# Kernel tuning notes

Measured on AMD Instinct MI355X. Metric: run time of the kernel, lower is better.

The kernel has to match this reference:

```python
import jax, jax.numpy as jnp
import numpy as np

D_MODEL = 512
EPS = 1e-5


def setup_inputs() -> dict:
    key = jax.random.key(0)
    k1, k2, k3 = jax.random.split(key, 3)
    B, N, D = 8, 2048, D_MODEL
    output = jax.random.normal(k1, (B, N, D), dtype=jnp.float32)
    # multiplicative 0/1 float mask over the [B, N, N] score matrix
    slf_attn_mask = jax.random.randint(k2, (B, N, N), 0, 2).astype(jnp.float32)
    # nn.Linear(d_model, d_model): weight [out, in], xavier-uniform; bias zeros-ish
    limit = float(np.sqrt(6.0 / (D + D)))
    W = jax.random.uniform(k3, (D, D), dtype=jnp.float32, minval=-limit, maxval=limit)
    b = jnp.zeros((D,), dtype=jnp.float32)
    return {"output": output, "slf_attn_mask": slf_attn_mask, "W": W, "b": b}


def reference(output, slf_attn_mask, W, b):
    temperature = jnp.asarray(D_MODEL, output.dtype) ** 0.5
    # scores: [B, N, N] = (q / temp) @ k^T, then multiplicative mask
    attn = jnp.einsum("bnd,bmd->bnm", output / temperature, output) * slf_attn_mask
    # F.normalize(p=2, dim=-1, eps=1e-5): x / max(||x||_2, eps)
    norm = jnp.sqrt(jnp.sum(attn * attn, axis=-1, keepdims=True))
    attn = attn / jnp.maximum(norm, EPS)
    # values: elu(Linear(output)), Linear uses W @ x + b with W [out, in]
    v = jax.nn.elu(jnp.einsum("bnd,ed->bne", output, W) + b)
    return jnp.einsum("bnm,bme->bne", attn, v)
```

## Files before the change

kernel.cpp:

```cpp
#include <hip/hip_runtime.h>
#include <hip/hip_bf16.h>

#define NSEQ 2048
#define DM 512
#define BATCH 8
#define GTOT (BATCH * NSEQ)
#define INV_T 0.044194173824159216f
#define EPSN 1e-5f

typedef __bf16 bf16_t;
typedef bf16_t bf16x8 __attribute__((ext_vector_type(8)));
typedef float f32x16 __attribute__((ext_vector_type(16)));
typedef unsigned short u16;
typedef unsigned int u32;
typedef unsigned long long u64;

__device__ __forceinline__ u16 f2bf(float f) {
    u32 u = __builtin_bit_cast(u32, f);
    u32 r = (u + 0x7FFFu + ((u >> 16) & 1u)) >> 16;
    return (u16)r;
}

__device__ __forceinline__ void async16(const u16* g, u16* l) {
    __builtin_amdgcn_global_load_lds(
        (const __attribute__((address_space(1))) u32*)g,
        (__attribute__((address_space(3))) u32*)l, 16, 0, 0);
}

__device__ __forceinline__ bf16x8 fragld64(const u16* t, int row, int kc) {
    return *(const bf16x8*)(t + row * 64 + ((kc ^ ((row >> 1) & 7)) << 3));
}

#define MFMA32(a, b, c) __builtin_amdgcn_mfma_f32_32x32x16_bf16(a, b, c, 0, 0, 0)
#define ROWOFF(reg, lh) (((reg) & 3) + 8 * ((reg) >> 2) + 4 * (lh))

#define STAGE64(Ag, ldA, Bg, ldB, k0)                                            \
    do {                                                                         \
        _Pragma("unroll") for (int j = 0; j < 4; ++j) {                          \
            const int cg = (lane & 7) ^ ((j * 4 + (lane >> 4)) & 7);             \
            const int dst = (wave * 4 + j) * 512 + lane * 8;                     \
            async16((Ag) + (long)(rS + j * 8) * (ldA) + (k0) + cg * 8, Ab + dst);\
            async16((Bg) + (long)(rS + j * 8) * (ldB) + (k0) + cg * 8, Bb + dst);\
        }                                                                        \
    } while (0)

__global__ __launch_bounds__(256) void k_convert(
    const float* __restrict__ X, const float* __restrict__ W,
    const float* __restrict__ mask, u16* __restrict__ Kbf, u16* __restrict__ Wbf,
    u64* __restrict__ Mbits, float* __restrict__ ssbuf) {
    const int bid = blockIdx.x;
    if (bid < 32768) {
        const int w = threadIdx.x >> 6, lane = threadIdx.x & 63;
        float4 f = ((const float4*)mask)[(long)bid * 256 + threadIdx.x];
        u64 b0 = __ballot(f.x != 0.f);
        u64 b1 = __ballot(f.y != 0.f);
        u64 b2 = __ballot(f.z != 0.f);
        u64 b3 = __ballot(f.w != 0.f);
        if (lane == 0) {
            u64* p = Mbits + ((long)bid * 4 + w) * 4;
            ((ulonglong2*)p)[0] = (ulonglong2){b0, b1};
            ((ulonglong2*)p)[1] = (ulonglong2){b2, b3};
        }
        return;
    }
    const long NK = (long)GTOT * DM / 4;
    const long NW = (long)DM * DM / 4;
    const long NS = GTOT / 4;
    long i = (long)(bid - 32768) * 256 + threadIdx.x;
    if (i < NK) {
        float4 f = ((const float4*)X)[i];
        ushort4 o;
        o.x = f2bf(f.x); o.y = f2bf(f.y); o.z = f2bf(f.z); o.w = f2bf(f.w);
        ((ushort4*)Kbf)[i] = o;
    } else if (i < NK + NW) {
        long j = i - NK;
        float4 f = ((const float4*)W)[j];
        ushort4 o;
        o.x = f2bf(f.x); o.y = f2bf(f.y); o.z = f2bf(f.z); o.w = f2bf(f.w);
        ((ushort4*)Wbf)[j] = o;
    } else if (i < NK + NW + NS) {
        ((float4*)ssbuf)[i - NK - NW] = (float4){0.f, 0.f, 0.f, 0.f};
    }
}

__global__ __launch_bounds__(256, 4) void k_sgemm(
    const u16* __restrict__ Kbf, const u64* __restrict__ Mbits,
    u16* __restrict__ Sbuf, float* __restrict__ ssbuf) {
    __shared__ __attribute__((aligned(16))) u16 Ab[8192], Bb[8192];
    const int tid = threadIdx.x, wave = tid >> 6, lane = tid & 63;
    const int l31 = lane & 31, lh = lane >> 5;
    const int wy = wave >> 1, wx = wave & 1;
    const int bid = blockIdx.x;
    const int b = bid & 7;
    const int ty = (bid >> 3) & 15, tx = bid >> 7;
    const int M0 = ty * 128, N0 = tx * 128;
    const u16* Ag = Kbf + (long)(b * NSEQ + M0) * DM;
    const u16* Bg = Kbf + (long)(b * NSEQ + N0) * DM;

    const int rS = wave * 32 + (lane >> 3);

    f32x16 acc[2][2];
#pragma unroll
    for (int i = 0; i < 2; ++i)
#pragma unroll
        for (int j = 0; j < 2; ++j)
#pragma unroll
            for (int e = 0; e < 16; ++e) acc[i][j][e] = 0.f;

    for (int kt = 0; kt < 8; ++kt) {
        const int k0 = kt * 64;
        __syncthreads();
        STAGE64(Ag, DM, Bg, DM, k0);
        __syncthreads();
#pragma unroll
        for (int ks = 0; ks < 4; ++ks) {
            const int kc = ks * 2 + lh;
            bf16x8 a0 = fragld64(Ab, wy * 64 + l31, kc);
            bf16x8 a1 = fragld64(Ab, wy * 64 + 32 + l31, kc);
            bf16x8 b0 = fragld64(Bb, wx * 64 + l31, kc);
            bf16x8 b1 = fragld64(Bb, wx * 64 + 32 + l31, kc);
            acc[0][0] = MFMA32(a0, b0, acc[0][0]);
            acc[0][1] = MFMA32(a0, b1, acc[0][1]);
            acc[1][0] = MFMA32(a1, b0, acc[1][0]);
            acc[1][1] = MFMA32(a1, b1, acc[1][1]);
        }
    }
#pragma unroll
    for (int mi = 0; mi < 2; ++mi) {
#pragma unroll
        for (int reg = 0; reg < 16; ++reg) {
            int rl = M0 + wy * 64 + mi * 32 + ROWOFF(reg, lh);
            long rg = (long)b * NSEQ + rl;
            const u64* Mr = Mbits + rg * 32;
            float v = 0.f;
#pragma unroll
            for (int ni = 0; ni < 2; ++ni) {
                int cg = N0 + wx * 64 + ni * 32 + l31;
                u64 wd = Mr[((cg >> 8) << 2) + (l31 & 3)];
                float s = ((wd >> ((cg >> 2) & 63)) & 1ull)
                              ? acc[mi][ni][reg] * INV_T : 0.f;
                v += s * s;
                Sbuf[rg * NSEQ + cg] = f2bf(s);
            }
            v += __shfl_xor(v, 1, 32);
            v += __shfl_xor(v, 2, 32);
            v += __shfl_xor(v, 4, 32);
            v += __shfl_xor(v, 8, 32);
            v += __shfl_xor(v, 16, 32);
            if (l31 == 0) atomicAdd(&ssbuf[rg], v);
        }
    }
}

__global__ __launch_bounds__(256, 4) void k_vgemm(
    const u16* __restrict__ Wbf, const u16* __restrict__ Kbf,
    const float* __restrict__ bias, u16* __restrict__ vT) {
    __shared__ __attribute__((aligned(16))) u16 Ab[8192], Bb[8192];
    const int tid = threadIdx.x, wave = tid >> 6, lane = tid & 63;
    const int l31 = lane & 31, lh = lane >> 5;
    const int wy = wave >> 1, wx = wave & 1;
    const int M0 = blockIdx.y * 128, N0 = blockIdx.x * 128;
    const u16* Ag = Wbf + (long)M0 * DM;
    const u16* Bg = Kbf + (long)N0 * DM;

    const int rS = wave * 32 + (lane >> 3);

    f32x16 acc[2][2];
#pragma unroll
    for (int i = 0; i < 2; ++i)
#pragma unroll
        for (int j = 0; j < 2; ++j)
#pragma unroll
            for (int e = 0; e < 16; ++e) acc[i][j][e] = 0.f;

    for (int kt = 0; kt < 8; ++kt) {
        const int k0 = kt * 64;
        __syncthreads();
        STAGE64(Ag, DM, Bg, DM, k0);
        __syncthreads();
#pragma unroll
        for (int ks = 0; ks < 4; ++ks) {
            const int kc = ks * 2 + lh;
            bf16x8 a0 = fragld64(Ab, wy * 64 + l31, kc);
            bf16x8 a1 = fragld64(Ab, wy * 64 + 32 + l31, kc);
            bf16x8 b0 = fragld64(Bb, wx * 64 + l31, kc);
            bf16x8 b1 = fragld64(Bb, wx * 64 + 32 + l31, kc);
            acc[0][0] = MFMA32(a0, b0, acc[0][0]);
            acc[0][1] = MFMA32(a0, b1, acc[0][1]);
            acc[1][0] = MFMA32(a1, b0, acc[1][0]);
            acc[1][1] = MFMA32(a1, b1, acc[1][1]);
        }
    }
#pragma unroll
    for (int mi = 0; mi < 2; ++mi) {
#pragma unroll
        for (int reg = 0; reg < 16; ++reg) {
            int e = M0 + wy * 64 + mi * 32 + ROWOFF(reg, lh);
            float bv = bias[e];
#pragma unroll
            for (int ni = 0; ni < 2; ++ni) {
                int g = N0 + wx * 64 + ni * 32 + l31;
                float x = acc[mi][ni][reg] + bv;
                float v = x > 0.f ? x : (__expf(x) - 1.f);
                vT[(long)e * GTOT + g] = f2bf(v);
            }
        }
    }
}

__global__ __launch_bounds__(256, 4) void k_pv(
    const u16* __restrict__ Sbuf, const u16* __restrict__ vT,
    const float* __restrict__ ssbuf, float* __restrict__ Out) {
    __shared__ __attribute__((aligned(16))) u16 Ab[8192], Bb[8192];
    __shared__ float sc[128];
    const int tid = threadIdx.x, wave = tid >> 6, lane = tid & 63;
    const int l31 = lane & 31, lh = lane >> 5;
    const int wy = wave >> 1, wx = wave & 1;
    const int bid = blockIdx.x;
    const int b = bid & 7;
    const int r = bid >> 3;
    const int tx = r & 3, ty = r >> 2;
    const int M0 = ty * 128, N0 = tx * 128;
    const u16* Ag = Sbuf + (long)(b * NSEQ + M0) * NSEQ;
    const u16* Bg = vT + (long)N0 * GTOT + b * NSEQ;

    if (tid < 128) {
        float v = ssbuf[b * NSEQ + M0 + tid];
        sc[tid] = 1.f / fmaxf(sqrtf(v), EPSN);
    }

    const int rS = wave * 32 + (lane >> 3);

    f32x16 acc[2][2];
#pragma unroll
    for (int i = 0; i < 2; ++i)
#pragma unroll
        for (int j = 0; j < 2; ++j)
#pragma unroll
            for (int e = 0; e < 16; ++e) acc[i][j][e] = 0.f;

    for (int kt = 0; kt < 32; ++kt) {
        const int k0 = kt * 64;
        __syncthreads();
        STAGE64(Ag, NSEQ, Bg, GTOT, k0);
        __syncthreads();
#pragma unroll
        for (int ks = 0; ks < 4; ++ks) {
            const int kc = ks * 2 + lh;
            bf16x8 a0 = fragld64(Ab, wy * 64 + l31, kc);
            bf16x8 a1 = fragld64(Ab, wy * 64 + 32 + l31, kc);
            bf16x8 b0 = fragld64(Bb, wx * 64 + l31, kc);
            bf16x8 b1 = fragld64(Bb, wx * 64 + 32 + l31, kc);
            acc[0][0] = MFMA32(a0, b0, acc[0][0]);
            acc[0][1] = MFMA32(a0, b1, acc[0][1]);
            acc[1][0] = MFMA32(a1, b0, acc[1][0]);
            acc[1][1] = MFMA32(a1, b1, acc[1][1]);
        }
    }
#pragma unroll
    for (int mi = 0; mi < 2; ++mi) {
#pragma unroll
        for (int reg = 0; reg < 16; ++reg) {
            int rl = wy * 64 + mi * 32 + ROWOFF(reg, lh);
            float s = sc[rl];
            float* op = Out + ((long)b * NSEQ + M0 + rl) * DM;
#pragma unroll
            for (int ni = 0; ni < 2; ++ni) {
                int d = N0 + wx * 64 + ni * 32 + l31;
                op[d] = acc[mi][ni][reg] * s;
            }
        }
    }
}

extern "C" void kernel_launch(void* const* d_in, const int* in_sizes, int n_in,
                              void* d_out, int out_size, void* d_ws, size_t ws_size,
                              hipStream_t stream) {
    const float* X = (const float*)d_in[0];
    const float* mask = (const float*)d_in[1];
    const float* W = (const float*)d_in[2];
    const float* bias = (const float*)d_in[3];
    float* out = (float*)d_out;

    char* ws = (char*)d_ws;
    u16* Kbf = (u16*)ws;
    u16* Wbf = (u16*)(ws + 16777216);
    u16* vT = (u16*)(ws + 17301504);
    u16* Sbuf = (u16*)(ws + 34078720);
    float* ssbuf = (float*)(ws + 101187584);
    u64* Mbits = (u64*)(ws + 101253120);

    k_convert<<<41232, 256, 0, stream>>>(X, W, mask, Kbf, Wbf, Mbits, ssbuf);
    k_vgemm<<<dim3(128, 4), 256, 0, stream>>>(Wbf, Kbf, bias, vT);
    k_sgemm<<<2048, 256, 0, stream>>>(Kbf, Mbits, Sbuf, ssbuf);
    k_pv<<<512, 256, 0, stream>>>(Sbuf, vT, ssbuf, out);
}
```

Measured before the change: 336.7 us.

## Merge V and score GEMMs into one launch; double-buffer PV kernel LDS

The value-projection GEMM and the masked score GEMM are merged into a single kernel whose first 512 blocks compute V and the rest compute scores. This removes one launch and lets the two independent GEMMs share the GPU. The PV kernel now uses two LDS buffers and issues the async load of the next K tile while computing the current one, with one barrier per tile instead of two. The double buffer doubles LDS use, so occupancy is lowered to 2 blocks per SM via launch bounds.

Result: no change. 337.9 us (+0.3%).

```diff
diff --git a/kernel.cpp b/kernel.cpp
--- a/kernel.cpp
+++ b/kernel.cpp
@@ -34,14 +34,14 @@
 #define MFMA32(a, b, c) __builtin_amdgcn_mfma_f32_32x32x16_bf16(a, b, c, 0, 0, 0)
 #define ROWOFF(reg, lh) (((reg) & 3) + 8 * ((reg) >> 2) + 4 * (lh))
 
-#define STAGE64(Ag, ldA, Bg, ldB, k0)                                            \
-    do {                                                                         \
-        _Pragma("unroll") for (int j = 0; j < 4; ++j) {                          \
-            const int cg = (lane & 7) ^ ((j * 4 + (lane >> 4)) & 7);             \
-            const int dst = (wave * 4 + j) * 512 + lane * 8;                     \
-            async16((Ag) + (long)(rS + j * 8) * (ldA) + (k0) + cg * 8, Ab + dst);\
-            async16((Bg) + (long)(rS + j * 8) * (ldB) + (k0) + cg * 8, Bb + dst);\
-        }                                                                        \
+#define STAGE64D(Ag, ldA, Bg, ldB, k0, Adst, Bdst)                                   \
+    do {                                                                             \
+        _Pragma("unroll") for (int j = 0; j < 4; ++j) {                              \
+            const int cg = (lane & 7) ^ ((j * 4 + (lane >> 4)) & 7);                 \
+            const int dst = (wave * 4 + j) * 512 + lane * 8;                         \
+            async16((Ag) + (long)(rS + j * 8) * (ldA) + (k0) + cg * 8, (Adst) + dst);\
+            async16((Bg) + (long)(rS + j * 8) * (ldB) + (k0) + cg * 8, (Bdst) + dst);\
+        }                                                                            \
     } while (0)
 
 __global__ __launch_bounds__(256) void k_convert(
@@ -83,34 +83,76 @@
     }
 }
 
-__global__ __launch_bounds__(256, 4) void k_sgemm(
+__global__ __launch_bounds__(256, 4) void k_work(
     const u16* __restrict__ Kbf, const u64* __restrict__ Mbits,
-    u16* __restrict__ Sbuf, float* __restrict__ ssbuf) {
+    const u16* __restrict__ Wbf, const float* __restrict__ bias,
+    u16* __restrict__ Sbuf, float* __restrict__ ssbuf, u16* __restrict__ vT) {
     __shared__ __attribute__((aligned(16))) u16 Ab[8192], Bb[8192];
     const int tid = threadIdx.x, wave = tid >> 6, lane = tid & 63;
     const int l31 = lane & 31, lh = lane >> 5;
     const int wy = wave >> 1, wx = wave & 1;
+    const int rS = wave * 32 + (lane >> 3);
     const int bid = blockIdx.x;
-    const int b = bid & 7;
-    const int ty = (bid >> 3) & 15, tx = bid >> 7;
+
+    f32x16 acc[2][2];
+#pragma unroll
+    for (int i = 0; i < 2; ++i)
+#pragma unroll
+        for (int j = 0; j < 2; ++j)
+#pragma unroll
+            for (int e = 0; e < 16; ++e) acc[i][j][e] = 0.f;
+
+    if (bid < 512) {
+        const int M0 = (bid & 3) * 128, N0 = (bid >> 2) * 128;
+        const u16* Ag = Wbf + (long)M0 * DM;
+        const u16* Bg = Kbf + (long)N0 * DM;
+
+        for (int kt = 0; kt < 8; ++kt) {
+            const int k0 = kt * 64;
+            __syncthreads();
+            STAGE64D(Ag, DM, Bg, DM, k0, Ab, Bb);
+            __syncthreads();
+#pragma unroll
+            for (int ks = 0; ks < 4; ++ks) {
+                const int kc = ks * 2 + lh;
+                bf16x8 a0 = fragld64(Ab, wy * 64 + l31, kc);
+                bf16x8 a1 = fragld64(Ab, wy * 64 + 32 + l31, kc);
+                bf16x8 b0 = fragld64(Bb, wx * 64 + l31, kc);
+                bf16x8 b1 = fragld64(Bb, wx * 64 + 32 + l31, kc);
+                acc[0][0] = MFMA32(a0, b0, acc[0][0]);
+                acc[0][1] = MFMA32(a0, b1, acc[0][1]);
+                acc[1][0] = MFMA32(a1, b0, acc[1][0]);
+                acc[1][1] = MFMA32(a1, b1, acc[1][1]);
+            }
+        }
+#pragma unroll
+        for (int mi = 0; mi < 2; ++mi) {
+#pragma unroll
+            for (int reg = 0; reg < 16; ++reg) {
+                int e = M0 + wy * 64 + mi * 32 + ROWOFF(reg, lh);
+                float bv = bias[e];
+#pragma unroll
+                for (int ni = 0; ni < 2; ++ni) {
+                    int g = N0 + wx * 64 + ni * 32 + l31;
+                    float x = acc[mi][ni][reg] + bv;
+                    float v = x > 0.f ? x : (__expf(x) - 1.f);
+                    vT[(long)e * GTOT + g] = f2bf(v);
+                }
+            }
+        }
+        return;
+    }
+    const int bs = bid - 512;
+    const int b = bs & 7;
+    const int ty = (bs >> 3) & 15, tx = bs >> 7;
     const int M0 = ty * 128, N0 = tx * 128;
     const u16* Ag = Kbf + (long)(b * NSEQ + M0) * DM;
     const u16* Bg = Kbf + (long)(b * NSEQ + N0) * DM;
 
-    const int rS = wave * 32 + (lane >> 3);
-
-    f32x16 acc[2][2];
-#pragma unroll
-    for (int i = 0; i < 2; ++i)
-#pragma unroll
-        for (int j = 0; j < 2; ++j)
-#pragma unroll
-            for (int e = 0; e < 16; ++e) acc[i][j][e] = 0.f;
-
     for (int kt = 0; kt < 8; ++kt) {
         const int k0 = kt * 64;
         __syncthreads();
-        STAGE64(Ag, DM, Bg, DM, k0);
+        STAGE64D(Ag, DM, Bg, DM, k0, Ab, Bb);
         __syncthreads();
 #pragma unroll
         for (int ks = 0; ks < 4; ++ks) {
@@ -152,66 +194,10 @@
     }
 }
 
-__global__ __launch_bounds__(256, 4) void k_vgemm(
-    const u16* __restrict__ Wbf, const u16* __restrict__ Kbf,
-    const float* __restrict__ bias, u16* __restrict__ vT) {
-    __shared__ __attribute__((aligned(16))) u16 Ab[8192], Bb[8192];
-    const int tid = threadIdx.x, wave = tid >> 6, lane = tid & 63;
-    const int l31 = lane & 31, lh = lane >> 5;
-    const int wy = wave >> 1, wx = wave & 1;
-    const int M0 = blockIdx.y * 128, N0 = blockIdx.x * 128;
-    const u16* Ag = Wbf + (long)M0 * DM;
-    const u16* Bg = Kbf + (long)N0 * DM;
-
-    const int rS = wave * 32 + (lane >> 3);
-
-    f32x16 acc[2][2];
-#pragma unroll
-    for (int i = 0; i < 2; ++i)
-#pragma unroll
-        for (int j = 0; j < 2; ++j)
-#pragma unroll
-            for (int e = 0; e < 16; ++e) acc[i][j][e] = 0.f;
-
-    for (int kt = 0; kt < 8; ++kt) {
-        const int k0 = kt * 64;
-        __syncthreads();
-        STAGE64(Ag, DM, Bg, DM, k0);
-        __syncthreads();
-#pragma unroll
-        for (int ks = 0; ks < 4; ++ks) {
-            const int kc = ks * 2 + lh;
-            bf16x8 a0 = fragld64(Ab, wy * 64 + l31, kc);
-            bf16x8 a1 = fragld64(Ab, wy * 64 + 32 + l31, kc);
-            bf16x8 b0 = fragld64(Bb, wx * 64 + l31, kc);
-            bf16x8 b1 = fragld64(Bb, wx * 64 + 32 + l31, kc);
-            acc[0][0] = MFMA32(a0, b0, acc[0][0]);
-            acc[0][1] = MFMA32(a0, b1, acc[0][1]);
-            acc[1][0] = MFMA32(a1, b0, acc[1][0]);
-            acc[1][1] = MFMA32(a1, b1, acc[1][1]);
-        }
-    }
-#pragma unroll
-    for (int mi = 0; mi < 2; ++mi) {
-#pragma unroll
-        for (int reg = 0; reg < 16; ++reg) {
-            int e = M0 + wy * 64 + mi * 32 + ROWOFF(reg, lh);
-            float bv = bias[e];
-#pragma unroll
-            for (int ni = 0; ni < 2; ++ni) {
-                int g = N0 + wx * 64 + ni * 32 + l31;
-                float x = acc[mi][ni][reg] + bv;
-                float v = x > 0.f ? x : (__expf(x) - 1.f);
-                vT[(long)e * GTOT + g] = f2bf(v);
-            }
-        }
-    }
-}
-
-__global__ __launch_bounds__(256, 4) void k_pv(
+__global__ __launch_bounds__(256, 2) void k_pv(
     const u16* __restrict__ Sbuf, const u16* __restrict__ vT,
     const float* __restrict__ ssbuf, float* __restrict__ Out) {
-    __shared__ __attribute__((aligned(16))) u16 Ab[8192], Bb[8192];
+    __shared__ __attribute__((aligned(16))) u16 A0[8192], B0[8192], A1[8192], B1[8192];
     __shared__ float sc[128];
     const int tid = threadIdx.x, wave = tid >> 6, lane = tid & 63;
     const int l31 = lane & 31, lh = lane >> 5;
@@ -223,14 +209,14 @@
     const int M0 = ty * 128, N0 = tx * 128;
     const u16* Ag = Sbuf + (long)(b * NSEQ + M0) * NSEQ;
     const u16* Bg = vT + (long)N0 * GTOT + b * NSEQ;
-
+    const int rS = wave * 32 + (lane >> 3);
+
+    STAGE64D(Ag, NSEQ, Bg, GTOT, 0, A0, B0);
     if (tid < 128) {
         float v = ssbuf[b * NSEQ + M0 + tid];
         sc[tid] = 1.f / fmaxf(sqrtf(v), EPSN);
     }
 
-    const int rS = wave * 32 + (lane >> 3);
-
     f32x16 acc[2][2];
 #pragma unroll
     for (int i = 0; i < 2; ++i)
@@ -239,24 +225,34 @@
 #pragma unroll
             for (int e = 0; e < 16; ++e) acc[i][j][e] = 0.f;
 
-    for (int kt = 0; kt < 32; ++kt) {
-        const int k0 = kt * 64;
-        __syncthreads();
-        STAGE64(Ag, NSEQ, Bg, GTOT, k0);
-        __syncthreads();
-#pragma unroll
-        for (int ks = 0; ks < 4; ++ks) {
-            const int kc = ks * 2 + lh;
-            bf16x8 a0 = fragld64(Ab, wy * 64 + l31, kc);
-            bf16x8 a1 = fragld64(Ab, wy * 64 + 32 + l31, kc);
-            bf16x8 b0 = fragld64(Bb, wx * 64 + l31, kc);
-            bf16x8 b1 = fragld64(Bb, wx * 64 + 32 + l31, kc);
-            acc[0][0] = MFMA32(a0, b0, acc[0][0]);
-            acc[0][1] = MFMA32(a0, b1, acc[0][1]);
-            acc[1][0] = MFMA32(a1, b0, acc[1][0]);
-            acc[1][1] = MFMA32(a1, b1, acc[1][1]);
-        }
-    }
+    __syncthreads();
+
+#define PVCOMP(Ac, Bc)                                                \
+    do {                                                              \
+        _Pragma("unroll") for (int ks = 0; ks < 4; ++ks) {            \
+            const int kc = ks * 2 + lh;                               \
+            bf16x8 a0 = fragld64((Ac), wy * 64 + l31, kc);            \
+            bf16x8 a1 = fragld64((Ac), wy * 64 + 32 + l31, kc);       \
+            bf16x8 b0 = fragld64((Bc), wx * 64 + l31, kc);            \
+            bf16x8 b1 = fragld64((Bc), wx * 64 + 32 + l31, kc);       \
+            acc[0][0] = MFMA32(a0, b0, acc[0][0]);                    \
+            acc[0][1] = MFMA32(a0, b1, acc[0][1]);                    \
+            acc[1][0] = MFMA32(a1, b0, acc[1][0]);                    \
+            acc[1][1] = MFMA32(a1, b1, acc[1][1]);                    \
+        }                                                             \
+    } while (0)
+
+    for (int t = 0; t < 16; ++t) {
+        const int k0 = t * 128;
+        STAGE64D(Ag, NSEQ, Bg, GTOT, k0 + 64, A1, B1);
+        PVCOMP(A0, B0);
+        __syncthreads();
+        if (t < 15) STAGE64D(Ag, NSEQ, Bg, GTOT, k0 + 128, A0, B0);
+        PVCOMP(A1, B1);
+        __syncthreads();
+    }
+#undef PVCOMP
+
 #pragma unroll
     for (int mi = 0; mi < 2; ++mi) {
 #pragma unroll
@@ -291,7 +287,6 @@
     u64* Mbits = (u64*)(ws + 101253120);
 
     k_convert<<<41232, 256, 0, stream>>>(X, W, mask, Kbf, Wbf, Mbits, ssbuf);
-    k_vgemm<<<dim3(128, 4), 256, 0, stream>>>(Wbf, Kbf, bias, vT);
-    k_sgemm<<<2048, 256, 0, stream>>>(Kbf, Mbits, Sbuf, ssbuf);
+    k_work<<<2560, 256, 0, stream>>>(Kbf, Mbits, Wbf, bias, Sbuf, ssbuf, vT);
     k_pv<<<512, 256, 0, stream>>>(Sbuf, vT, ssbuf, out);
 }
```

## Exploit score symmetry, merge V-gemm into score kernel, grid-stride convert kernel

Applied to the files above, without the earlier changes.

The score GEMM now computes only upper-triangular tiles of X·X^T, because the unmasked scores are symmetric. For off-diagonal tiles it also writes the transposed tile, masked with the transposed mask bits, to Sbuf, which roughly halves the score MFMA work. The V projection GEMM is folded into the same launch as the first 512 blocks, removing one kernel launch and letting the two GEMMs overlap. The conversion kernel is changed from one element per thread across 41k blocks to a fixed 2048-block loop over elements, and the transposed stores use lane shuffles to build packed 16-byte writes. The cost is extra epilogue work and scattered row-norm atomics in the transposed path.

Measured after the change: 335.7 us. About the same (-0.3%).

```diff
diff --git a/kernel.cpp b/kernel.cpp
--- a/kernel.cpp
+++ b/kernel.cpp
@@ -48,64 +48,108 @@
     const float* __restrict__ X, const float* __restrict__ W,
     const float* __restrict__ mask, u16* __restrict__ Kbf, u16* __restrict__ Wbf,
     u64* __restrict__ Mbits, float* __restrict__ ssbuf) {
-    const int bid = blockIdx.x;
-    if (bid < 32768) {
-        const int w = threadIdx.x >> 6, lane = threadIdx.x & 63;
-        float4 f = ((const float4*)mask)[(long)bid * 256 + threadIdx.x];
+    const int gtid = blockIdx.x * 256 + threadIdx.x;
+    const int lane = threadIdx.x & 63;
+    const float4* m4 = (const float4*)mask;
+#pragma unroll
+    for (int it = 0; it < 16; ++it) {
+        long idx = (long)it * 524288 + gtid;
+        float4 f = m4[idx];
         u64 b0 = __ballot(f.x != 0.f);
         u64 b1 = __ballot(f.y != 0.f);
         u64 b2 = __ballot(f.z != 0.f);
         u64 b3 = __ballot(f.w != 0.f);
         if (lane == 0) {
-            u64* p = Mbits + ((long)bid * 4 + w) * 4;
+            u64* p = Mbits + ((idx >> 6) << 2);
             ((ulonglong2*)p)[0] = (ulonglong2){b0, b1};
             ((ulonglong2*)p)[1] = (ulonglong2){b2, b3};
         }
-        return;
-    }
-    const long NK = (long)GTOT * DM / 4;
-    const long NW = (long)DM * DM / 4;
-    const long NS = GTOT / 4;
-    long i = (long)(bid - 32768) * 256 + threadIdx.x;
-    if (i < NK) {
+    }
+#pragma unroll
+    for (int it = 0; it < 4; ++it) {
+        long i = (long)it * 524288 + gtid;
         float4 f = ((const float4*)X)[i];
         ushort4 o;
         o.x = f2bf(f.x); o.y = f2bf(f.y); o.z = f2bf(f.z); o.w = f2bf(f.w);
         ((ushort4*)Kbf)[i] = o;
-    } else if (i < NK + NW) {
-        long j = i - NK;
-        float4 f = ((const float4*)W)[j];
+    }
+    if (gtid < 65536) {
+        float4 f = ((const float4*)W)[gtid];
         ushort4 o;
         o.x = f2bf(f.x); o.y = f2bf(f.y); o.z = f2bf(f.z); o.w = f2bf(f.w);
-        ((ushort4*)Wbf)[j] = o;
-    } else if (i < NK + NW + NS) {
-        ((float4*)ssbuf)[i - NK - NW] = (float4){0.f, 0.f, 0.f, 0.f};
-    }
-}
-
-__global__ __launch_bounds__(256, 4) void k_sgemm(
+        ((ushort4*)Wbf)[gtid] = o;
+    }
+    if (gtid < 4096) ((float4*)ssbuf)[gtid] = (float4){0.f, 0.f, 0.f, 0.f};
+}
+
+__global__ __launch_bounds__(256, 4) void k_work(
     const u16* __restrict__ Kbf, const u64* __restrict__ Mbits,
-    u16* __restrict__ Sbuf, float* __restrict__ ssbuf) {
+    const u16* __restrict__ Wbf, const float* __restrict__ bias,
+    u16* __restrict__ Sbuf, float* __restrict__ ssbuf, u16* __restrict__ vT) {
     __shared__ __attribute__((aligned(16))) u16 Ab[8192], Bb[8192];
     const int tid = threadIdx.x, wave = tid >> 6, lane = tid & 63;
     const int l31 = lane & 31, lh = lane >> 5;
     const int wy = wave >> 1, wx = wave & 1;
+    const int rS = wave * 32 + (lane >> 3);
     const int bid = blockIdx.x;
-    const int b = bid & 7;
-    const int ty = (bid >> 3) & 15, tx = bid >> 7;
+
+    f32x16 acc[2][2];
+#pragma unroll
+    for (int i = 0; i < 2; ++i)
+#pragma unroll
+        for (int j = 0; j < 2; ++j)
+#pragma unroll
+            for (int e = 0; e < 16; ++e) acc[i][j][e] = 0.f;
+
+    if (bid < 512) {
+        const int M0 = (bid & 3) * 128, N0 = (bid >> 2) * 128;
+        const u16* Ag = Wbf + (long)M0 * DM;
+        const u16* Bg = Kbf + (long)N0 * DM;
+
+        for (int kt = 0; kt < 8; ++kt) {
+            const int k0 = kt * 64;
+            __syncthreads();
+            STAGE64(Ag, DM, Bg, DM, k0);
+            __syncthreads();
+#pragma unroll
+            for (int ks = 0; ks < 4; ++ks) {
+                const int kc = ks * 2 + lh;
+                bf16x8 a0 = fragld64(Ab, wy * 64 + l31, kc);
+                bf16x8 a1 = fragld64(Ab, wy * 64 + 32 + l31, kc);
+                bf16x8 b0 = fragld64(Bb, wx * 64 + l31, kc);
+                bf16x8 b1 = fragld64(Bb, wx * 64 + 32 + l31, kc);
+                acc[0][0] = MFMA32(a0, b0, acc[0][0]);
+                acc[0][1] = MFMA32(a0, b1, acc[0][1]);
+                acc[1][0] = MFMA32(a1, b0, acc[1][0]);
+                acc[1][1] = MFMA32(a1, b1, acc[1][1]);
+            }
+        }
+#pragma unroll
+        for (int mi = 0; mi < 2; ++mi) {
+#pragma unroll
+            for (int reg = 0; reg < 16; ++reg) {
+                int e = M0 + wy * 64 + mi * 32 + ROWOFF(reg, lh);
+                float bv = bias[e];
+#pragma unroll
+                for (int ni = 0; ni < 2; ++ni) {
+                    int g = N0 + wx * 64 + ni * 32 + l31;
+                    float x = acc[mi][ni][reg] + bv;
+                    float v = x > 0.f ? x : (__expf(x) - 1.f);
+                    vT[(long)e * GTOT + g] = f2bf(v);
+                }
+            }
+        }
+        return;
+    }
+    const int bs = bid - 512;
+    const int b = bs & 7;
+    int t = bs >> 3;
+    int ty = 0;
+    while (t >= 16 - ty) { t -= 16 - ty; ++ty; }
+    const int tx = ty + t;
     const int M0 = ty * 128, N0 = tx * 128;
     const u16* Ag = Kbf + (long)(b * NSEQ + M0) * DM;
     const u16* Bg = Kbf + (long)(b * NSEQ + N0) * DM;
-
-    const int rS = wave * 32 + (lane >> 3);
-
-    f32x16 acc[2][2];
-#pragma unroll
-    for (int i = 0; i < 2; ++i)
-#pragma unroll
-        for (int j = 0; j < 2; ++j)
-#pragma unroll
-            for (int e = 0; e < 16; ++e) acc[i][j][e] = 0.f;
 
     for (int kt = 0; kt < 8; ++kt) {
         const int k0 = kt * 64;
@@ -150,60 +194,46 @@
             if (l31 == 0) atomicAdd(&ssbuf[rg], v);
         }
     }
-}
-
-__global__ __launch_bounds__(256, 4) void k_vgemm(
-    const u16* __restrict__ Wbf, const u16* __restrict__ Kbf,
-    const float* __restrict__ bias, u16* __restrict__ vT) {
-    __shared__ __attribute__((aligned(16))) u16 Ab[8192], Bb[8192];
-    const int tid = threadIdx.x, wave = tid >> 6, lane = tid & 63;
-    const int l31 = lane & 31, lh = lane >> 5;
-    const int wy = wave >> 1, wx = wave & 1;
-    const int M0 = blockIdx.y * 128, N0 = blockIdx.x * 128;
-    const u16* Ag = Wbf + (long)M0 * DM;
-    const u16* Bg = Kbf + (long)N0 * DM;
-
-    const int rS = wave * 32 + (lane >> 3);
-
-    f32x16 acc[2][2];
-#pragma unroll
-    for (int i = 0; i < 2; ++i)
-#pragma unroll
-        for (int j = 0; j < 2; ++j)
-#pragma unroll
-            for (int e = 0; e < 16; ++e) acc[i][j][e] = 0.f;
-
-    for (int kt = 0; kt < 8; ++kt) {
-        const int k0 = kt * 64;
-        __syncthreads();
-        STAGE64(Ag, DM, Bg, DM, k0);
-        __syncthreads();
-#pragma unroll
-        for (int ks = 0; ks < 4; ++ks) {
-            const int kc = ks * 2 + lh;
-            bf16x8 a0 = fragld64(Ab, wy * 64 + l31, kc);
-            bf16x8 a1 = fragld64(Ab, wy * 64 + 32 + l31, kc);
-            bf16x8 b0 = fragld64(Bb, wx * 64 + l31, kc);
-            bf16x8 b1 = fragld64(Bb, wx * 64 + 32 + l31, kc);
-            acc[0][0] = MFMA32(a0, b0, acc[0][0]);
-            acc[0][1] = MFMA32(a0, b1, acc[0][1]);
-            acc[1][0] = MFMA32(a1, b0, acc[1][0]);
-            acc[1][1] = MFMA32(a1, b1, acc[1][1]);
-        }
-    }
-#pragma unroll
-    for (int mi = 0; mi < 2; ++mi) {
-#pragma unroll
-        for (int reg = 0; reg < 16; ++reg) {
-            int e = M0 + wy * 64 + mi * 32 + ROWOFF(reg, lh);
-            float bv = bias[e];
-#pragma unroll
-            for (int ni = 0; ni < 2; ++ni) {
-                int g = N0 + wx * 64 + ni * 32 + l31;
-                float x = acc[mi][ni][reg] + bv;
-                float v = x > 0.f ? x : (__expf(x) - 1.f);
-                vT[(long)e * GTOT + g] = f2bf(v);
-            }
+    if (ty != tx) {
+        const int c0 = M0 + wy * 64;
+        const int wb = (c0 >> 8) << 2;
+        const int bb = (c0 >> 2) & 63;
+#pragma unroll
+        for (int ni = 0; ni < 2; ++ni) {
+            const long Rg = (long)b * NSEQ + N0 + wx * 64 + ni * 32 + l31;
+            const u64* Mr = Mbits + Rg * 32 + wb;
+            u64 mw0 = Mr[0], mw1 = Mr[1], mw2 = Mr[2], mw3 = Mr[3];
+            u16* orow = Sbuf + Rg * NSEQ + c0;
+            float ssm = 0.f;
+#pragma unroll
+            for (int k2 = 0; k2 < 4; ++k2) {
+                u16 v0[4], v1[4];
+#pragma unroll
+                for (int i = 0; i < 4; ++i) {
+                    u64 w = (i == 0) ? mw0 : (i == 1) ? mw1 : (i == 2) ? mw2 : mw3;
+                    const int bit0 = bb + 2 * k2 + lh;
+                    const int bit1 = bit0 + 8;
+                    float s0 = ((w >> bit0) & 1ull) ? acc[0][ni][4 * k2 + i] * INV_T : 0.f;
+                    float s1 = ((w >> bit1) & 1ull) ? acc[1][ni][4 * k2 + i] * INV_T : 0.f;
+                    ssm += s0 * s0 + s1 * s1;
+                    v0[i] = f2bf(s0);
+                    v1[i] = f2bf(s1);
+                }
+                u32 p0lo = v0[0] | ((u32)v0[1] << 16), p0hi = v0[2] | ((u32)v0[3] << 16);
+                u32 p1lo = v1[0] | ((u32)v1[1] << 16), p1hi = v1[2] | ((u32)v1[3] << 16);
+                u32 send0 = lh ? p0lo : p1lo, send1 = lh ? p0hi : p1hi;
+                u32 own0 = lh ? p1lo : p0lo, own1 = lh ? p1hi : p0hi;
+                u32 r0 = (u32)__shfl_xor((int)send0, 32);
+                u32 r1 = (u32)__shfl_xor((int)send1, 32);
+                uint4 st;
+                st.x = lh ? r0 : own0;
+                st.y = lh ? r1 : own1;
+                st.z = lh ? own0 : r0;
+                st.w = lh ? own1 : r1;
+                *(uint4*)(orow + 8 * (k2 + 4 * lh)) = st;
+            }
+            ssm += __shfl_xor(ssm, 32);
+            if (lh == 0) atomicAdd(&ssbuf[Rg], ssm);
         }
     }
 }
@@ -290,8 +320,7 @@
     float* ssbuf = (float*)(ws + 101187584);
     u64* Mbits = (u64*)(ws + 101253120);
 
-    k_convert<<<41232, 256, 0, stream>>>(X, W, mask, Kbf, Wbf, Mbits, ssbuf);
-    k_vgemm<<<dim3(128, 4), 256, 0, stream>>>(Wbf, Kbf, bias, vT);
-    k_sgemm<<<2048, 256, 0, stream>>>(Kbf, Mbits, Sbuf, ssbuf);
+    k_convert<<<2048, 256, 0, stream>>>(X, W, mask, Kbf, Wbf, Mbits, ssbuf);
+    k_work<<<1600, 256, 0, stream>>>(Kbf, Mbits, Wbf, bias, Sbuf, ssbuf, vT);
     k_pv<<<512, 256, 0, stream>>>(Sbuf, vT, ssbuf, out);
 }
```
